# Performance work log

Hardware: AMD Instinct MI355X
Metric: run time of the kernel (lower is better)

The kernel has to match this reference:

```python
import jax, jax.numpy as jnp
import numpy as np

C = 512
CQK = C // 8  # 64


def setup_inputs() -> dict:
    key = jax.random.key(0)
    ks = jax.random.split(key, 8)
    B, H, W = 16, 32, 32
    x = jax.random.normal(ks[0], (B, C, H, W), dtype=jnp.float32)
    # 1x1 conv weights stored as [out_ch, in_ch] matrices + biases
    sq = 1.0 / np.sqrt(C)
    Wq = jax.random.uniform(ks[1], (CQK, C), jnp.float32, -sq, sq)
    bq = jax.random.uniform(ks[2], (CQK,), jnp.float32, -sq, sq)
    Wk = jax.random.uniform(ks[3], (CQK, C), jnp.float32, -sq, sq)
    bk = jax.random.uniform(ks[4], (CQK,), jnp.float32, -sq, sq)
    Wv = jax.random.uniform(ks[5], (C, C), jnp.float32, -sq, sq)
    bv = jax.random.uniform(ks[6], (C,), jnp.float32, -sq, sq)
    gamma = jax.random.normal(ks[7], (1,), dtype=jnp.float32)
    return {"x": x, "Wq": Wq, "bq": bq, "Wk": Wk, "bk": bk, "Wv": Wv, "bv": bv, "gamma": gamma}


def reference(x, Wq, bq, Wk, bk, Wv, bv, gamma):
    B, Cin, H, W = x.shape
    xf = x.reshape(B, Cin, H * W)  # [B, C, N]
    # 1x1 convs == channel matmuls
    q = jnp.einsum('qc,bcn->bnq', Wq, xf) + bq[None, None, :]   # [B, N, Cqk]
    k = jnp.einsum('qc,bcn->bqn', Wk, xf) + bk[None, :, None]   # [B, Cqk, N]
    v = jnp.einsum('vc,bcn->bvn', Wv, xf) + bv[None, :, None]   # [B, C, N]
    scores = jnp.einsum('bnq,bqm->bnm', q, k)                    # [B, N, N]
    attn = jax.nn.softmax(scores, axis=-1)                       # softmax over keys
    # values @ attn^T : out[b,c,n] = sum_m v[b,c,m] * attn[b,n,m]
    attended = jnp.einsum('bvm,bnm->bvn', v, attn)               # [B, C, N]
    attended = attended.reshape(B, Cin, H, W)
    return gamma[0] * attended + x
```

## Files before the change

kernel.cpp:

```cpp
#include <hip/hip_runtime.h>
#include <stdint.h>

#define BB 16
#define CC 512
#define CQK 64
#define NN 1024

typedef __attribute__((ext_vector_type(8))) short bf16x8;
typedef __attribute__((ext_vector_type(4))) short short4v;
typedef __attribute__((ext_vector_type(8))) unsigned short ushort8;
typedef __attribute__((ext_vector_type(4))) float f32x4;

static __device__ __forceinline__ unsigned short f2bf(float f) {
  uint32_t u = __float_as_uint(f);
  u += 0x7FFFu + ((u >> 16) & 1u);
  return (unsigned short)(u >> 16);
}

static __device__ __forceinline__ void gll16(const unsigned short* g, unsigned short* l) {
  const __attribute__((address_space(1))) unsigned int* gp =
      reinterpret_cast<const __attribute__((address_space(1))) unsigned int*>(
          reinterpret_cast<uintptr_t>(g));
  __attribute__((address_space(3))) unsigned int* lp =
      reinterpret_cast<__attribute__((address_space(3))) unsigned int*>(
          (unsigned int)reinterpret_cast<uintptr_t>(l));
  __builtin_amdgcn_global_load_lds(gp, lp, 16, 0, 0);
}

__global__ __launch_bounds__(256) void k_pack_w(
    const float* __restrict__ Wq, const float* __restrict__ Wk,
    const float* __restrict__ Wv, unsigned short* __restrict__ Wall) {
  int idx = blockIdx.x * 256 + threadIdx.x;
  int e = idx * 4;
  if (e >= 640 * 512) return;
  int o = e >> 9;
  int c = e & 511;
  const float* src;
  if (o < 64)        src = Wq + (size_t)o * 512;
  else if (o < 128)  src = Wk + (size_t)(o - 64) * 512;
  else               src = Wv + (size_t)(o - 128) * 512;
  float4 v = *(const float4*)(src + c);
  short4v pk;
  pk[0] = (short)f2bf(v.x); pk[1] = (short)f2bf(v.y);
  pk[2] = (short)f2bf(v.z); pk[3] = (short)f2bf(v.w);
  *(short4v*)(Wall + e) = pk;
}

__global__ __launch_bounds__(256) void k_transpose_x(
    const float* __restrict__ x, unsigned short* __restrict__ xT) {
  __shared__ float tile[32][33];
  int b = blockIdx.z;
  int c0 = blockIdx.y * 32;
  int n0 = blockIdx.x * 32;
  int t = threadIdx.x;
  int tn = t & 31, tc = t >> 5;
  const float* xp = x + ((size_t)b * CC + c0) * NN + n0;
#pragma unroll
  for (int i = 0; i < 4; i++) {
    int c = tc + i * 8;
    tile[c][tn] = xp[(size_t)c * NN + tn];
  }
  __syncthreads();
  unsigned short* xq = xT + ((size_t)b * NN + n0) * CC + c0;
  int n = t >> 3;
  int cq = (t & 7) * 4;
  short4v pk;
#pragma unroll
  for (int k = 0; k < 4; k++) pk[k] = (short)f2bf(tile[cq + k][n]);
  *(short4v*)(&xq[(size_t)n * CC + cq]) = pk;
}

__global__ __launch_bounds__(256) void k_gemm1(
    const unsigned short* __restrict__ Wall, const unsigned short* __restrict__ xT,
    const float* __restrict__ bq, const float* __restrict__ bk,
    const float* __restrict__ bv,
    unsigned short* __restrict__ qkT, unsigned short* __restrict__ vbuf) {
  __shared__ __align__(16) unsigned short ldsA[128 * 32];
  __shared__ __align__(16) unsigned short ldsB[128 * 32];
  int b = blockIdx.z;
  int o0 = blockIdx.y * 128;
  int n0 = blockIdx.x * 128;
  int t = threadIdx.x;
  int w = t >> 6, l = t & 63;
  int wm = w & 1, wn = w >> 1;
  int lr = l & 15, lq = l >> 4;

  f32x4 acc[4][4];
#pragma unroll
  for (int i = 0; i < 4; i++)
#pragma unroll
    for (int j = 0; j < 4; j++) acc[i][j] = (f32x4){0.f, 0.f, 0.f, 0.f};

  const unsigned short* Ab = Wall + (size_t)o0 * CC;
  const unsigned short* Bb = xT + ((size_t)b * NN + n0) * CC;
  int srow = t >> 2;
  int skq = (t & 3) * 8;
  int ldsw = (t >> 6) * 512;

  for (int kt = 0; kt < CC; kt += 32) {
#pragma unroll
    for (int p = 0; p < 2; p++) {
      int r = p * 64 + srow;
      gll16(&Ab[(size_t)r * CC + kt + skq], &ldsA[p * 2048 + ldsw]);
      gll16(&Bb[(size_t)r * CC + kt + skq], &ldsB[p * 2048 + ldsw]);
    }
    __syncthreads();
    bf16x8 af[4], bfr[4];
#pragma unroll
    for (int i = 0; i < 4; i++)
      af[i] = *(const bf16x8*)(&ldsA[(wm * 64 + i * 16 + lr) * 32 + lq * 8]);
#pragma unroll
    for (int j = 0; j < 4; j++)
      bfr[j] = *(const bf16x8*)(&ldsB[(wn * 64 + j * 16 + lr) * 32 + lq * 8]);
#pragma unroll
    for (int i = 0; i < 4; i++)
#pragma unroll
      for (int j = 0; j < 4; j++)
        acc[i][j] = __builtin_amdgcn_mfma_f32_16x16x32_bf16(af[i], bfr[j], acc[i][j], 0, 0, 0);
    __syncthreads();
  }

  if (o0 == 0) {
#pragma unroll
    for (int i = 0; i < 4; i++) {
      int ob = wm * 64 + i * 16 + lq * 4;
#pragma unroll
      for (int j = 0; j < 4; j++) {
        int n = n0 + wn * 64 + j * 16 + lr;
        short4v pk;
#pragma unroll
        for (int r = 0; r < 4; r++) {
          int o = ob + r;
          float bias = (o < 64) ? bq[o] : bk[o - 64];
          pk[r] = (short)f2bf(acc[i][j][r] + bias);
        }
        *(short4v*)(&qkT[((size_t)b * NN + n) * 128 + ob]) = pk;
      }
    }
  } else {
#pragma unroll
    for (int i = 0; i < 4; i++) {
#pragma unroll
      for (int r = 0; r < 4; r++) {
        int o = o0 + wm * 64 + i * 16 + lq * 4 + r;
        int c = o - 128;
        float bias = bv[c];
#pragma unroll
        for (int j = 0; j < 4; j++) {
          int n = n0 + wn * 64 + j * 16 + lr;
          vbuf[((size_t)b * CC + c) * NN + n] = f2bf(acc[i][j][r] + bias);
        }
      }
    }
  }
}

#define QT 64
#define MC 64
#define PSTR 72

__global__ __launch_bounds__(256, 2) void k_flash(
    const unsigned short* __restrict__ qkT, const unsigned short* __restrict__ vbuf,
    const float* __restrict__ x, const float* __restrict__ gamma,
    float* __restrict__ out) {
  __shared__ __align__(16) unsigned short P[QT * PSTR];
  __shared__ float red[4 * QT];
  __shared__ float fin[QT];

  int b = blockIdx.z;
  int chalf = blockIdx.y;
  int n0 = blockIdx.x * QT;
  int t = threadIdx.x;
  int w = t >> 6, l = t & 63;
  int lr = l & 15, lq = l >> 4;
  const unsigned short* qk = qkT + (size_t)b * NN * 128;
  const unsigned short* Vb = vbuf + ((size_t)b * CC + chalf * 256 + w * 64) * NN;

  bf16x8 aq[4][2];
#pragma unroll
  for (int nj = 0; nj < 4; nj++)
#pragma unroll
    for (int ks = 0; ks < 2; ks++)
      aq[nj][ks] = *(const bf16x8*)(&qk[(size_t)(n0 + nj * 16 + lr) * 128 + ks * 32 + lq * 8]);

  f32x4 acc[4][4];
#pragma unroll
  for (int ci = 0; ci < 4; ci++)
#pragma unroll
    for (int nj = 0; nj < 4; nj++) acc[ci][nj] = (f32x4){0.f, 0.f, 0.f, 0.f};
  float sreg[4][4];
#pragma unroll
  for (int nj = 0; nj < 4; nj++)
#pragma unroll
    for (int r = 0; r < 4; r++) sreg[nj][r] = 0.f;

  float ev[4][4];
  {
    int mrow = w * 16 + lr;
    bf16x8 kf0 = *(const bf16x8*)(&qk[(size_t)mrow * 128 + 64 + lq * 8]);
    bf16x8 kf1 = *(const bf16x8*)(&qk[(size_t)mrow * 128 + 96 + lq * 8]);
#pragma unroll
    for (int nj = 0; nj < 4; nj++) {
      f32x4 s = (f32x4){0.f, 0.f, 0.f, 0.f};
      s = __builtin_amdgcn_mfma_f32_16x16x32_bf16(aq[nj][0], kf0, s, 0, 0, 0);
      s = __builtin_amdgcn_mfma_f32_16x16x32_bf16(aq[nj][1], kf1, s, 0, 0, 0);
#pragma unroll
      for (int r = 0; r < 4; r++) {
        float e = __expf(s[r]);
        ev[nj][r] = e;
        sreg[nj][r] += e;
      }
    }
  }

  for (int m0 = 0; m0 < NN; m0 += MC) {
    bf16x8 af0[4];
#pragma unroll
    for (int ci = 0; ci < 4; ci++)
      af0[ci] = *(const bf16x8*)(&Vb[(size_t)(ci * 16 + lr) * NN + m0 + lq * 8]);

    __syncthreads();
#pragma unroll
    for (int nj = 0; nj < 4; nj++)
#pragma unroll
      for (int r = 0; r < 4; r++)
        P[(nj * 16 + lq * 4 + r) * PSTR + w * 16 + lr] = f2bf(ev[nj][r]);

    if (m0 + MC < NN) {
      int mrow = m0 + MC + w * 16 + lr;
      bf16x8 kf0 = *(const bf16x8*)(&qk[(size_t)mrow * 128 + 64 + lq * 8]);
      bf16x8 kf1 = *(const bf16x8*)(&qk[(size_t)mrow * 128 + 96 + lq * 8]);
#pragma unroll
      for (int nj = 0; nj < 4; nj++) {
        f32x4 s = (f32x4){0.f, 0.f, 0.f, 0.f};
        s = __builtin_amdgcn_mfma_f32_16x16x32_bf16(aq[nj][0], kf0, s, 0, 0, 0);
        s = __builtin_amdgcn_mfma_f32_16x16x32_bf16(aq[nj][1], kf1, s, 0, 0, 0);
#pragma unroll
        for (int r = 0; r < 4; r++) {
          float e = __expf(s[r]);
          ev[nj][r] = e;
          sreg[nj][r] += e;
        }
      }
    }
    __syncthreads();

    bf16x8 af1[4];
#pragma unroll
    for (int ci = 0; ci < 4; ci++)
      af1[ci] = *(const bf16x8*)(&Vb[(size_t)(ci * 16 + lr) * NN + m0 + 32 + lq * 8]);

#pragma unroll
    for (int nj = 0; nj < 4; nj++) {
      bf16x8 pf = *(const bf16x8*)(&P[(nj * 16 + lr) * PSTR + lq * 8]);
#pragma unroll
      for (int ci = 0; ci < 4; ci++)
        acc[ci][nj] = __builtin_amdgcn_mfma_f32_16x16x32_bf16(af0[ci], pf, acc[ci][nj], 0, 0, 0);
    }
#pragma unroll
    for (int nj = 0; nj < 4; nj++) {
      bf16x8 pf = *(const bf16x8*)(&P[(nj * 16 + lr) * PSTR + 32 + lq * 8]);
#pragma unroll
      for (int ci = 0; ci < 4; ci++)
        acc[ci][nj] = __builtin_amdgcn_mfma_f32_16x16x32_bf16(af1[ci], pf, acc[ci][nj], 0, 0, 0);
    }
  }

#pragma unroll
  for (int nj = 0; nj < 4; nj++)
#pragma unroll
    for (int r = 0; r < 4; r++) {
#pragma unroll
      for (int d = 1; d < 16; d <<= 1) sreg[nj][r] += __shfl_xor(sreg[nj][r], d, 64);
    }
  __syncthreads();
  if (lr == 0) {
#pragma unroll
    for (int nj = 0; nj < 4; nj++)
#pragma unroll
      for (int r = 0; r < 4; r++) red[w * QT + nj * 16 + lq * 4 + r] = sreg[nj][r];
  }
  __syncthreads();
  if (t < QT) {
    float ssum = red[t] + red[QT + t] + red[2 * QT + t] + red[3 * QT + t];
    fin[t] = ssum;
  }
  __syncthreads();

  float invL[4];
#pragma unroll
  for (int nj = 0; nj < 4; nj++) invL[nj] = 1.0f / fin[nj * 16 + lr];
  float g = gamma[0];
#pragma unroll
  for (int ci = 0; ci < 4; ci++) {
#pragma unroll
    for (int r = 0; r < 4; r++) {
      int c = chalf * 256 + w * 64 + ci * 16 + lq * 4 + r;
#pragma unroll
      for (int nj = 0; nj < 4; nj++) {
        size_t idx = ((size_t)b * CC + c) * NN + n0 + nj * 16 + lr;
        out[idx] = g * acc[ci][nj][r] * invL[nj] + x[idx];
      }
    }
  }
}

extern "C" void kernel_launch(void* const* d_in, const int* in_sizes, int n_in,
                              void* d_out, int out_size, void* d_ws, size_t ws_size,
                              hipStream_t stream) {
  (void)in_sizes; (void)n_in; (void)out_size; (void)ws_size;
  const float* x     = (const float*)d_in[0];
  const float* Wq    = (const float*)d_in[1];
  const float* bq    = (const float*)d_in[2];
  const float* Wk    = (const float*)d_in[3];
  const float* bk    = (const float*)d_in[4];
  const float* Wv    = (const float*)d_in[5];
  const float* bv    = (const float*)d_in[6];
  const float* gamma = (const float*)d_in[7];
  float* out = (float*)d_out;

  char* ws = (char*)d_ws;
  unsigned short* Wall = (unsigned short*)(ws);
  unsigned short* xT   = (unsigned short*)(ws + 655360);
  unsigned short* qkT  = (unsigned short*)(ws + 655360 + 16777216);
  unsigned short* vbuf = (unsigned short*)(ws + 655360 + 16777216 + 4194304);

  k_pack_w<<<dim3(320), dim3(256), 0, stream>>>(Wq, Wk, Wv, Wall);
  k_transpose_x<<<dim3(NN / 32, CC / 32, BB), dim3(256), 0, stream>>>(x, xT);
  k_gemm1<<<dim3(NN / 128, 640 / 128, BB), dim3(256), 0, stream>>>(Wall, xT, bq, bk, bv, qkT, vbuf);
  k_flash<<<dim3(NN / QT, 2, BB), dim3(256), 0, stream>>>(qkT, vbuf, x, gamma, out);
}
```

Baseline: 169.5 us.

## Split flash kernel into channel quarters with double-buffered P and higher occupancy

The attention kernel now splits output channels into four quarters instead of two, which doubles the grid to 1024 blocks and halves each wave's accumulator registers. Launch bounds are raised to allow 4 blocks per CU. P is double-buffered in LDS, so one barrier per chunk is dropped, and blocks are linearised so that neighbouring blocks share a batch and query tile for L2 reuse of K/Q. The trade-off is that the QK^T scores and exp are recomputed twice as many times across channel groups.

```diff
diff --git a/kernel.cpp b/kernel.cpp
--- a/kernel.cpp
+++ b/kernel.cpp
@@ -159,22 +159,25 @@
 #define MC 64
 #define PSTR 72
 
-__global__ __launch_bounds__(256, 2) void k_flash(
+__global__ __launch_bounds__(256, 4) void k_flash(
     const unsigned short* __restrict__ qkT, const unsigned short* __restrict__ vbuf,
     const float* __restrict__ x, const float* __restrict__ gamma,
     float* __restrict__ out) {
-  __shared__ __align__(16) unsigned short P[QT * PSTR];
+  __shared__ __align__(16) unsigned short P[2][QT * PSTR];
   __shared__ float red[4 * QT];
   __shared__ float fin[QT];
 
-  int b = blockIdx.z;
-  int chalf = blockIdx.y;
-  int n0 = blockIdx.x * QT;
+  int lin = blockIdx.x;
+  int ntile = lin >> 6;
+  int rem = lin & 63;
+  int b = rem >> 2;
+  int cq = rem & 3;
+  int n0 = ntile * QT;
   int t = threadIdx.x;
   int w = t >> 6, l = t & 63;
   int lr = l & 15, lq = l >> 4;
   const unsigned short* qk = qkT + (size_t)b * NN * 128;
-  const unsigned short* Vb = vbuf + ((size_t)b * CC + chalf * 256 + w * 64) * NN;
+  const unsigned short* Vb = vbuf + ((size_t)b * CC + cq * 128 + w * 32) * NN;
 
   bf16x8 aq[4][2];
 #pragma unroll
@@ -183,9 +186,9 @@
     for (int ks = 0; ks < 2; ks++)
       aq[nj][ks] = *(const bf16x8*)(&qk[(size_t)(n0 + nj * 16 + lr) * 128 + ks * 32 + lq * 8]);
 
-  f32x4 acc[4][4];
-#pragma unroll
-  for (int ci = 0; ci < 4; ci++)
+  f32x4 acc[2][4];
+#pragma unroll
+  for (int ci = 0; ci < 2; ci++)
 #pragma unroll
     for (int nj = 0; nj < 4; nj++) acc[ci][nj] = (f32x4){0.f, 0.f, 0.f, 0.f};
   float sreg[4][4];
@@ -213,20 +216,16 @@
     }
   }
 
-  for (int m0 = 0; m0 < NN; m0 += MC) {
-    bf16x8 af0[4];
-#pragma unroll
-    for (int ci = 0; ci < 4; ci++)
-      af0[ci] = *(const bf16x8*)(&Vb[(size_t)(ci * 16 + lr) * NN + m0 + lq * 8]);
-
-    __syncthreads();
+  for (int ch = 0; ch < NN / MC; ch++) {
+    int m0 = ch * MC;
+    unsigned short* Pb = P[ch & 1];
 #pragma unroll
     for (int nj = 0; nj < 4; nj++)
 #pragma unroll
       for (int r = 0; r < 4; r++)
-        P[(nj * 16 + lq * 4 + r) * PSTR + w * 16 + lr] = f2bf(ev[nj][r]);
-
-    if (m0 + MC < NN) {
+        Pb[(nj * 16 + lq * 4 + r) * PSTR + w * 16 + lr] = f2bf(ev[nj][r]);
+
+    if (ch + 1 < NN / MC) {
       int mrow = m0 + MC + w * 16 + lr;
       bf16x8 kf0 = *(const bf16x8*)(&qk[(size_t)mrow * 128 + 64 + lq * 8]);
       bf16x8 kf1 = *(const bf16x8*)(&qk[(size_t)mrow * 128 + 96 + lq * 8]);
@@ -243,27 +242,25 @@
         }
       }
     }
+
+    bf16x8 af[2][2];
+#pragma unroll
+    for (int ci = 0; ci < 2; ci++)
+#pragma unroll
+      for (int ks = 0; ks < 2; ks++)
+        af[ci][ks] = *(const bf16x8*)(&Vb[(size_t)(ci * 16 + lr) * NN + m0 + ks * 32 + lq * 8]);
+
     __syncthreads();
 
-    bf16x8 af1[4];
-#pragma unroll
-    for (int ci = 0; ci < 4; ci++)
-      af1[ci] = *(const bf16x8*)(&Vb[(size_t)(ci * 16 + lr) * NN + m0 + 32 + lq * 8]);
-
-#pragma unroll
-    for (int nj = 0; nj < 4; nj++) {
-      bf16x8 pf = *(const bf16x8*)(&P[(nj * 16 + lr) * PSTR + lq * 8]);
-#pragma unroll
-      for (int ci = 0; ci < 4; ci++)
-        acc[ci][nj] = __builtin_amdgcn_mfma_f32_16x16x32_bf16(af0[ci], pf, acc[ci][nj], 0, 0, 0);
-    }
-#pragma unroll
-    for (int nj = 0; nj < 4; nj++) {
-      bf16x8 pf = *(const bf16x8*)(&P[(nj * 16 + lr) * PSTR + 32 + lq * 8]);
-#pragma unroll
-      for (int ci = 0; ci < 4; ci++)
-        acc[ci][nj] = __builtin_amdgcn_mfma_f32_16x16x32_bf16(af1[ci], pf, acc[ci][nj], 0, 0, 0);
-    }
+#pragma unroll
+    for (int ks = 0; ks < 2; ks++)
+#pragma unroll
+      for (int nj = 0; nj < 4; nj++) {
+        bf16x8 pf = *(const bf16x8*)(&Pb[(nj * 16 + lr) * PSTR + ks * 32 + lq * 8]);
+#pragma unroll
+        for (int ci = 0; ci < 2; ci++)
+          acc[ci][nj] = __builtin_amdgcn_mfma_f32_16x16x32_bf16(af[ci][ks], pf, acc[ci][nj], 0, 0, 0);
+      }
   }
 
 #pragma unroll
@@ -282,8 +279,7 @@
   }
   __syncthreads();
   if (t < QT) {
-    float ssum = red[t] + red[QT + t] + red[2 * QT + t] + red[3 * QT + t];
-    fin[t] = ssum;
+    fin[t] = red[t] + red[QT + t] + red[2 * QT + t] + red[3 * QT + t];
   }
   __syncthreads();
 
@@ -292,10 +288,10 @@
   for (int nj = 0; nj < 4; nj++) invL[nj] = 1.0f / fin[nj * 16 + lr];
   float g = gamma[0];
 #pragma unroll
-  for (int ci = 0; ci < 4; ci++) {
+  for (int ci = 0; ci < 2; ci++) {
 #pragma unroll
     for (int r = 0; r < 4; r++) {
-      int c = chalf * 256 + w * 64 + ci * 16 + lq * 4 + r;
+      int c = cq * 128 + w * 32 + ci * 16 + lq * 4 + r;
 #pragma unroll
       for (int nj = 0; nj < 4; nj++) {
         size_t idx = ((size_t)b * CC + c) * NN + n0 + nj * 16 + lr;
@@ -328,5 +324,5 @@
   k_pack_w<<<dim3(320), dim3(256), 0, stream>>>(Wq, Wk, Wv, Wall);
   k_transpose_x<<<dim3(NN / 32, CC / 32, BB), dim3(256), 0, stream>>>(x, xT);
   k_gemm1<<<dim3(NN / 128, 640 / 128, BB), dim3(256), 0, stream>>>(Wall, xT, bq, bk, bv, qkT, vbuf);
-  k_flash<<<dim3(NN / QT, 2, BB), dim3(256), 0, stream>>>(qkT, vbuf, x, gamma, out);
-}
+  k_flash<<<dim3((NN / QT) * 4 * BB), dim3(256), 0, stream>>>(qkT, vbuf, x, gamma, out);
+}
```

After: 184.0 us. +8.6%, slower.
